# Optimization experiments

Hardware: AMD Instinct MI355X
Metric: run time of the kernel (lower is better)

The kernel has to match this reference:

```python
import jax, jax.numpy as jnp
import numpy as np


def _sample_plane(plane, coords):
    """torch.nn.functional.grid_sample, mode='bilinear', padding_mode='zeros',
    align_corners=True.  plane: [C,H,W]; coords: [N,2] with (x,y) in [-1,1]
    (x indexes W, y indexes H, as in torch grid convention).  Returns [N,C]."""
    C, H, W = plane.shape
    x = (coords[:, 0] + 1.0) * 0.5 * (W - 1)
    y = (coords[:, 1] + 1.0) * 0.5 * (H - 1)
    x0f = jnp.floor(x); y0f = jnp.floor(y)
    wx = x - x0f; wy = y - y0f

    def corner(yi, xi):
        valid = (xi >= 0) & (xi < W) & (yi >= 0) & (yi < H)
        xc = jnp.clip(xi, 0, W - 1).astype(jnp.int32)
        yc = jnp.clip(yi, 0, H - 1).astype(jnp.int32)
        return plane[:, yc, xc] * valid.astype(plane.dtype)  # [C,N]

    v00 = corner(y0f, x0f)
    v01 = corner(y0f, x0f + 1)
    v10 = corner(y0f + 1, x0f)
    v11 = corner(y0f + 1, x0f + 1)
    out = (v00 * (1 - wx) * (1 - wy) + v01 * wx * (1 - wy)
           + v10 * (1 - wx) * wy + v11 * wx * wy)
    return out.T  # [N,C]


_sample_batched = jax.vmap(_sample_plane)  # [B,C,H,W],[B,N,2] -> [B,N,C]


def setup_inputs() -> dict:
    key = jax.random.key(0)
    ks = jax.random.split(key, 8)
    B, N, C, R = 4, 131072, 32, 256
    triplanes = jax.random.normal(ks[0], (B, 3, C, R, R), jnp.float32) * 0.1
    coordinates = jax.random.uniform(ks[1], (B, N, 3), jnp.float32, -1.0, 1.0)
    # MLP weights ~ frequency_init(30) / first_layer_sine_init scales
    w0 = jax.random.uniform(ks[2], (128, C), jnp.float32, -1.0 / C, 1.0 / C)
    b0 = jnp.zeros((128,), jnp.float32)
    s1 = np.sqrt(6.0 / 128) / 30.0
    w1 = jax.random.uniform(ks[3], (128, 128), jnp.float32, -s1, s1)
    b1 = jnp.zeros((128,), jnp.float32)
    w2 = jax.random.uniform(ks[4], (1, 128), jnp.float32, -s1, s1)
    b2 = jnp.zeros((1,), jnp.float32)
    return {"triplanes": triplanes, "coordinates": coordinates,
            "w0": w0, "b0": b0, "w1": w1, "b1": b1, "w2": w2, "b2": b2}


def reference(triplanes, coordinates, w0, b0, w1, b1, w2, b2):
    # triplanes: [B,3,C,R,R]; coordinates: [B,N,3]
    xy = _sample_batched(triplanes[:, 0], coordinates[..., 0:2])   # (x,y)
    yz = _sample_batched(triplanes[:, 1], coordinates[..., 1:3])   # (y,z)
    xz = _sample_batched(triplanes[:, 2], coordinates[..., 0::2])  # (x,z)
    features = xy * yz * xz  # aggregate_fn == 'prod'; [B,N,C]
    h = jax.nn.relu(jnp.einsum('bnc,hc->bnh', features, w0) + b0)
    h = jax.nn.relu(jnp.einsum('bnh,gh->bng', h, w1) + b1)
    return jnp.einsum('bng,og->bno', h, w2) + b2  # [B,N,1]
```

## Files before the change

kernel.cpp:

```cpp
#include <hip/hip_runtime.h>
#include <hip/hip_bf16.h>
#include <cstddef>

#define RES 256
#define NCH 32
#define NPT 131072
#define NB  4

typedef _Float16 half8 __attribute__((ext_vector_type(8)));
typedef _Float16 half4 __attribute__((ext_vector_type(4)));
typedef float    f32x4 __attribute__((ext_vector_type(4)));

#define FEAT_STRIDE 40
#define H0_STRIDE   136
#define WAVE_LDS    (32 * H0_STRIDE)

__global__ __launch_bounds__(256) void transpose_prep_kernel(
    const float* __restrict__ in,
    const float* __restrict__ w0, const float* __restrict__ w1,
    _Float16* __restrict__ out,
    _Float16* __restrict__ w0h, _Float16* __restrict__ w1h)
{
    const int bp = blockIdx.y;
    const int t  = threadIdx.x;

    if (bp == 12) {
        const int i = blockIdx.x * 256 + t;
        if (i < 128 * NCH)  w0h[i] = (_Float16)(w0[i] * 16.0f);
        if (i < 128 * 128)  w1h[i] = (_Float16)w1[i];
        return;
    }

    __shared__ _Float16 tileh[NCH][RES + 8];
    const int y = blockIdx.x;

    const float4* src4 = (const float4*)(in + (size_t)bp * NCH * RES * RES);
    const int lane64 = t & 63;
    const int cq     = t >> 6;
    #pragma unroll
    for (int i = 0; i < 8; ++i) {
        const int c = cq * 8 + i;
        const float4 v = src4[(size_t)c * (RES * RES / 4) + y * (RES / 4) + lane64];
        half4 h = { (_Float16)v.x, (_Float16)v.y, (_Float16)v.z, (_Float16)v.w };
        *(half4*)&tileh[c][lane64 * 4] = h;
    }
    __syncthreads();

    _Float16* dst = out + ((size_t)bp * RES * RES + (size_t)y * RES) * NCH;
    const int x = t;
    #pragma unroll
    for (int cg = 0; cg < 4; ++cg) {
        half8 h;
        #pragma unroll
        for (int k = 0; k < 8; ++k)
            h[k] = tileh[cg * 8 + k][x];
        *(half8*)&dst[(size_t)x * NCH + cg * 8] = h;
    }
}

__global__ __launch_bounds__(64, 1) void fused_kernel(
    const _Float16* __restrict__ planesT,
    const float* __restrict__ coords,
    const _Float16* __restrict__ w0h,
    const _Float16* __restrict__ w1h,
    const float* __restrict__ b0, const float* __restrict__ b1,
    const float* __restrict__ w2, const float* __restrict__ b2,
    float* __restrict__ out)
{
    __shared__ __align__(16) _Float16 wbase[WAVE_LDS];

    const int tid  = threadIdx.x;
    const int l15  = tid & 15;
    const int quad = tid >> 4;

    {
        const int p  = tid >> 1;
        const int hf = tid & 1;
        const int gp = blockIdx.x * 32 + p;
        const int b  = gp >> 17;
        const float cx = coords[(size_t)gp * 3 + 0];
        const float cy = coords[(size_t)gp * 3 + 1];
        const float cz = coords[(size_t)gp * 3 + 2];

        int   offs[12];
        float wgt[12];
        #pragma unroll
        for (int pl = 0; pl < 3; ++pl) {
            const float u = (pl == 0) ? cx : (pl == 1) ? cy : cx;
            const float v = (pl == 0) ? cy : cz;

            const float fx = (u + 1.0f) * 0.5f * (RES - 1);
            const float fy = (v + 1.0f) * 0.5f * (RES - 1);
            const float x0f = floorf(fx), y0f = floorf(fy);
            const float wx = fx - x0f, wy = fy - y0f;
            const int x0 = (int)x0f, y0 = (int)y0f;
            const bool vx1 = (x0 + 1) < RES;
            const bool vy1 = (y0 + 1) < RES;
            const int x1 = vx1 ? x0 + 1 : RES - 1;
            const int y1 = vy1 ? y0 + 1 : RES - 1;

            float w00 = (1.0f - wx) * (1.0f - wy);
            float w01 = wx * (1.0f - wy);
            float w10 = (1.0f - wx) * wy;
            float w11 = wx * wy;
            if (!vx1) { w01 = 0.0f; w11 = 0.0f; }
            if (!vy1) { w10 = 0.0f; w11 = 0.0f; }

            const int pbase = ((b * 3 + pl) << 21) + (hf << 4);
            offs[pl * 4 + 0] = pbase + (y0 << 13) + (x0 << 5);
            offs[pl * 4 + 1] = pbase + (y0 << 13) + (x1 << 5);
            offs[pl * 4 + 2] = pbase + (y1 << 13) + (x0 << 5);
            offs[pl * 4 + 3] = pbase + (y1 << 13) + (x1 << 5);
            wgt[pl * 4 + 0] = w00; wgt[pl * 4 + 1] = w01;
            wgt[pl * 4 + 2] = w10; wgt[pl * 4 + 3] = w11;
        }

        __builtin_amdgcn_sched_barrier(0);
        half8 L0[12], L1[12];
        #pragma unroll
        for (int i = 0; i < 12; ++i) {
            const _Float16* cp = planesT + (size_t)(unsigned)offs[i];
            L0[i] = *(const half8*)cp;
            L1[i] = *(const half8*)(cp + 8);
        }
        __builtin_amdgcn_sched_barrier(0);

        float prod[16];
        #pragma unroll
        for (int pl = 0; pl < 3; ++pl) {
            #pragma unroll
            for (int k = 0; k < 8; ++k) {
                const float t0 =
                    fmaf((float)L0[pl*4+3][k], wgt[pl*4+3],
                    fmaf((float)L0[pl*4+2][k], wgt[pl*4+2],
                    fmaf((float)L0[pl*4+1][k], wgt[pl*4+1],
                         (float)L0[pl*4+0][k] * wgt[pl*4+0])));
                const float t1 =
                    fmaf((float)L1[pl*4+3][k], wgt[pl*4+3],
                    fmaf((float)L1[pl*4+2][k], wgt[pl*4+2],
                    fmaf((float)L1[pl*4+1][k], wgt[pl*4+1],
                         (float)L1[pl*4+0][k] * wgt[pl*4+0])));
                if (pl == 0) { prod[k] = t0;  prod[8 + k] = t1; }
                else         { prod[k] *= t0; prod[8 + k] *= t1; }
            }
        }

        half8 o0, o1;
        #pragma unroll
        for (int k = 0; k < 8; ++k) {
            o0[k] = (_Float16)(prod[k]     * 256.0f);
            o1[k] = (_Float16)(prod[8 + k] * 256.0f);
        }
        *(half8*)&wbase[p * FEAT_STRIDE + hf * 16 + 0] = o0;
        *(half8*)&wbase[p * FEAT_STRIDE + hf * 16 + 8] = o1;
    }

    half8 a0[2];
    #pragma unroll
    for (int mt = 0; mt < 2; ++mt)
        a0[mt] = *(const half8*)&wbase[(mt * 16 + l15) * FEAT_STRIDE + quad * 8];

    float b0v[8], b1v[8], w2s[8];
    #pragma unroll
    for (int nt = 0; nt < 8; ++nt) {
        b0v[nt] = b0[nt * 16 + l15] * 4096.0f;
        b1v[nt] = b1[nt * 16 + l15] * 4096.0f;
        w2s[nt] = w2[nt * 16 + l15] * (1.0f / 4096.0f);
    }

    #pragma unroll 1
    for (int nt = 0; nt < 8; ++nt) {
        const half8 bfr = *(const half8*)&w0h[(nt * 16 + l15) * NCH + quad * 8];
        f32x4 acc[2];
        #pragma unroll
        for (int mt = 0; mt < 2; ++mt) {
            acc[mt] = (f32x4){0.f, 0.f, 0.f, 0.f};
            acc[mt] = __builtin_amdgcn_mfma_f32_16x16x32_f16(
                a0[mt], bfr, acc[mt], 0, 0, 0);
        }
        #pragma unroll
        for (int mt = 0; mt < 2; ++mt)
            #pragma unroll
            for (int r = 0; r < 4; ++r) {
                const float hval = fmaxf(acc[mt][r] + b0v[nt], 0.0f);
                wbase[(mt * 16 + quad * 4 + r) * H0_STRIDE + nt * 16 + l15]
                    = (_Float16)hval;
            }
    }

    half8 a1[2][4];
    #pragma unroll
    for (int mt = 0; mt < 2; ++mt)
        #pragma unroll
        for (int ks = 0; ks < 4; ++ks)
            a1[mt][ks] = *(const half8*)
                &wbase[(mt * 16 + l15) * H0_STRIDE + ks * 32 + quad * 8];

    float part[2][4];
    #pragma unroll
    for (int mt = 0; mt < 2; ++mt)
        #pragma unroll
        for (int r = 0; r < 4; ++r) part[mt][r] = 0.0f;

    #pragma unroll 2
    for (int nt = 0; nt < 8; ++nt) {
        f32x4 acc[2];
        #pragma unroll
        for (int mt = 0; mt < 2; ++mt) acc[mt] = (f32x4){0.f, 0.f, 0.f, 0.f};
        #pragma unroll
        for (int ks = 0; ks < 4; ++ks) {
            const half8 bfr = *(const half8*)
                &w1h[(nt * 16 + l15) * 128 + ks * 32 + quad * 8];
            #pragma unroll
            for (int mt = 0; mt < 2; ++mt)
                acc[mt] = __builtin_amdgcn_mfma_f32_16x16x32_f16(
                    a1[mt][ks], bfr, acc[mt], 0, 0, 0);
        }
        #pragma unroll
        for (int mt = 0; mt < 2; ++mt)
            #pragma unroll
            for (int r = 0; r < 4; ++r)
                part[mt][r] = fmaf(w2s[nt], fmaxf(acc[mt][r] + b1v[nt], 0.0f),
                                   part[mt][r]);
    }

    #pragma unroll
    for (int mt = 0; mt < 2; ++mt)
        #pragma unroll
        for (int r = 0; r < 4; ++r) {
            float s = part[mt][r];
            s += __shfl_xor(s, 1);
            s += __shfl_xor(s, 2);
            s += __shfl_xor(s, 4);
            s += __shfl_xor(s, 8);
            part[mt][r] = s;
        }

    if (l15 == 0) {
        const float bias2 = b2[0];
        const int base = blockIdx.x * 32;
        #pragma unroll
        for (int mt = 0; mt < 2; ++mt)
            #pragma unroll
            for (int r = 0; r < 4; ++r)
                out[base + mt * 16 + quad * 4 + r] = part[mt][r] + bias2;
    }
}

__global__ __launch_bounds__(256) void fused_fallback(
    const float* __restrict__ planes, const float* __restrict__ coords,
    const float* __restrict__ w0, const float* __restrict__ b0,
    const float* __restrict__ w1, const float* __restrict__ b1,
    const float* __restrict__ w2, const float* __restrict__ b2,
    float* __restrict__ out)
{
    const int t = blockIdx.x * 256 + threadIdx.x;
    const int b = t >> 17;
    const float cx = coords[(size_t)t * 3 + 0];
    const float cy = coords[(size_t)t * 3 + 1];
    const float cz = coords[(size_t)t * 3 + 2];
    float feat[NCH];
    #pragma unroll
    for (int p = 0; p < 3; ++p) {
        const float u = (p == 0) ? cx : (p == 1) ? cy : cx;
        const float v = (p == 0) ? cy : cz;
        const float fx = (u + 1.0f) * 0.5f * (RES - 1);
        const float fy = (v + 1.0f) * 0.5f * (RES - 1);
        const float x0f = floorf(fx), y0f = floorf(fy);
        const float wx = fx - x0f, wy = fy - y0f;
        const int x0 = (int)x0f, y0 = (int)y0f;
        const bool vx1 = (x0 + 1) < RES, vy1 = (y0 + 1) < RES;
        const int x1 = vx1 ? x0 + 1 : RES - 1;
        const int y1 = vy1 ? y0 + 1 : RES - 1;
        float w00 = (1.0f - wx) * (1.0f - wy), w01 = wx * (1.0f - wy);
        float w10 = (1.0f - wx) * wy, w11 = wx * wy;
        if (!vx1) { w01 = 0.0f; w11 = 0.0f; }
        if (!vy1) { w10 = 0.0f; w11 = 0.0f; }
        const float* base = planes + (size_t)(b * 3 + p) * NCH * RES * RES;
        const float* p00 = base + (size_t)y0 * RES + x0;
        const float* p01 = base + (size_t)y0 * RES + x1;
        const float* p10 = base + (size_t)y1 * RES + x0;
        const float* p11 = base + (size_t)y1 * RES + x1;
        #pragma unroll
        for (int c = 0; c < NCH; ++c) {
            const size_t off = (size_t)c * RES * RES;
            float s = p00[off] * w00;
            s = fmaf(p01[off], w01, s);
            s = fmaf(p10[off], w10, s);
            s = fmaf(p11[off], w11, s);
            if (p == 0) feat[c] = s; else feat[c] *= s;
        }
    }
    float h0[128];
    #pragma unroll
    for (int g = 0; g < 128; ++g) {
        const float* wr = w0 + g * NCH;
        float aA = b0[g], aB = 0.0f;
        #pragma unroll
        for (int c = 0; c < NCH; c += 2) {
            aA = fmaf(wr[c], feat[c], aA);
            aB = fmaf(wr[c + 1], feat[c + 1], aB);
        }
        h0[g] = fmaxf(aA + aB, 0.0f);
    }
    float o = b2[0];
    for (int g = 0; g < 128; ++g) {
        const float* wr = w1 + g * 128;
        float aA = b1[g], aB = 0.0f, aC = 0.0f, aD = 0.0f;
        #pragma unroll
        for (int h = 0; h < 128; h += 4) {
            aA = fmaf(wr[h], h0[h], aA);
            aB = fmaf(wr[h + 1], h0[h + 1], aB);
            aC = fmaf(wr[h + 2], h0[h + 2], aC);
            aD = fmaf(wr[h + 3], h0[h + 3], aD);
        }
        o = fmaf(fmaxf((aA + aB) + (aC + aD), 0.0f), w2[g], o);
    }
    out[t] = o;
}

extern "C" void kernel_launch(void* const* d_in, const int* in_sizes, int n_in,
                              void* d_out, int out_size, void* d_ws, size_t ws_size,
                              hipStream_t stream)
{
    const float* trip   = (const float*)d_in[0];
    const float* coords = (const float*)d_in[1];
    const float* w0     = (const float*)d_in[2];
    const float* b0     = (const float*)d_in[3];
    const float* w1     = (const float*)d_in[4];
    const float* b1     = (const float*)d_in[5];
    const float* w2     = (const float*)d_in[6];
    const float* b2     = (const float*)d_in[7];
    float* out = (float*)d_out;

    const size_t planesTBytes = (size_t)NB * 3 * RES * RES * NCH * 2;
    const size_t w0hBytes = 128 * NCH * 2;
    const size_t w1hBytes = 128 * 128 * 2;
    const size_t needed = planesTBytes + w0hBytes + w1hBytes;

    if (ws_size >= needed) {
        _Float16* planesT = (_Float16*)d_ws;
        _Float16* w0h     = (_Float16*)((char*)d_ws + planesTBytes);
        _Float16* w1h     = (_Float16*)((char*)d_ws + planesTBytes + w0hBytes);

        transpose_prep_kernel<<<dim3(RES, NB * 3 + 1), 256, 0, stream>>>(
            trip, w0, w1, planesT, w0h, w1h);
        fused_kernel<<<(NB * NPT) / 32, 64, 0, stream>>>(
            planesT, coords, w0h, w1h, b0, b1, w2, b2, out);
    } else {
        fused_fallback<<<(NB * NPT) / 256, 256, 0, stream>>>(
            trip, coords, w0, b0, w1, b1, w2, b2, out);
    }
}
```

Before: 275.3 us.

## Split per-block points into two 16-point groups and overlap gathers with MLP

Each 64-thread block now handles its 32 points as two groups of 16, with 4 lanes per point loading 8 channels each instead of 2 lanes loading 16. Gathers for both groups are issued before the first group's interpolation and MLP, so the second group's loads can overlap compute on the first. LDS use is halved, which may help occupancy. The trade-off is that the MLP runs as single-M-tile MFMA passes, so weight fragments are reloaded twice and there is less MFMA instruction-level parallelism per pass.

Result: slower. 336.5 us (+22.2%).

```diff
diff --git a/kernel.cpp b/kernel.cpp
--- a/kernel.cpp
+++ b/kernel.cpp
@@ -13,7 +13,6 @@
 
 #define FEAT_STRIDE 40
 #define H0_STRIDE   136
-#define WAVE_LDS    (32 * H0_STRIDE)
 
 __global__ __launch_bounds__(256) void transpose_prep_kernel(
     const float* __restrict__ in,
@@ -67,23 +66,29 @@
     const float* __restrict__ w2, const float* __restrict__ b2,
     float* __restrict__ out)
 {
-    __shared__ __align__(16) _Float16 wbase[WAVE_LDS];
+    __shared__ __align__(16) _Float16 wbase[16 * H0_STRIDE];
 
     const int tid  = threadIdx.x;
     const int l15  = tid & 15;
     const int quad = tid >> 4;
-
-    {
-        const int p  = tid >> 1;
-        const int hf = tid & 1;
-        const int gp = blockIdx.x * 32 + p;
+    const int p    = tid >> 2;
+    const int hf2  = tid & 3;
+
+    float b0v[8], b1v[8], w2s[8];
+    #pragma unroll
+    for (int nt = 0; nt < 8; ++nt) {
+        b0v[nt] = b0[nt * 16 + l15] * 4096.0f;
+        b1v[nt] = b1[nt * 16 + l15] * 4096.0f;
+        w2s[nt] = w2[nt * 16 + l15] * (1.0f / 4096.0f);
+    }
+    const float bias2 = b2[0];
+
+    auto computeAddr = [&](int g, int* offs, float* wgt) {
+        const int gp = blockIdx.x * 32 + g * 16 + p;
         const int b  = gp >> 17;
         const float cx = coords[(size_t)gp * 3 + 0];
         const float cy = coords[(size_t)gp * 3 + 1];
         const float cz = coords[(size_t)gp * 3 + 2];
-
-        int   offs[12];
-        float wgt[12];
         #pragma unroll
         for (int pl = 0; pl < 3; ++pl) {
             const float u = (pl == 0) ? cx : (pl == 1) ? cy : cx;
@@ -106,7 +111,7 @@
             if (!vx1) { w01 = 0.0f; w11 = 0.0f; }
             if (!vy1) { w10 = 0.0f; w11 = 0.0f; }
 
-            const int pbase = ((b * 3 + pl) << 21) + (hf << 4);
+            const int pbase = ((b * 3 + pl) << 21) + hf2 * 8;
             offs[pl * 4 + 0] = pbase + (y0 << 13) + (x0 << 5);
             offs[pl * 4 + 1] = pbase + (y0 << 13) + (x1 << 5);
             offs[pl * 4 + 2] = pbase + (y1 << 13) + (x0 << 5);
@@ -114,137 +119,103 @@
             wgt[pl * 4 + 0] = w00; wgt[pl * 4 + 1] = w01;
             wgt[pl * 4 + 2] = w10; wgt[pl * 4 + 3] = w11;
         }
-
-        __builtin_amdgcn_sched_barrier(0);
-        half8 L0[12], L1[12];
-        #pragma unroll
-        for (int i = 0; i < 12; ++i) {
-            const _Float16* cp = planesT + (size_t)(unsigned)offs[i];
-            L0[i] = *(const half8*)cp;
-            L1[i] = *(const half8*)(cp + 8);
-        }
-        __builtin_amdgcn_sched_barrier(0);
-
-        float prod[16];
+    };
+
+    auto interpStore = [&](const half8* L, const float* wgt) {
+        float prod[8];
         #pragma unroll
         for (int pl = 0; pl < 3; ++pl) {
             #pragma unroll
             for (int k = 0; k < 8; ++k) {
                 const float t0 =
-                    fmaf((float)L0[pl*4+3][k], wgt[pl*4+3],
-                    fmaf((float)L0[pl*4+2][k], wgt[pl*4+2],
-                    fmaf((float)L0[pl*4+1][k], wgt[pl*4+1],
-                         (float)L0[pl*4+0][k] * wgt[pl*4+0])));
-                const float t1 =
-                    fmaf((float)L1[pl*4+3][k], wgt[pl*4+3],
-                    fmaf((float)L1[pl*4+2][k], wgt[pl*4+2],
-                    fmaf((float)L1[pl*4+1][k], wgt[pl*4+1],
-                         (float)L1[pl*4+0][k] * wgt[pl*4+0])));
-                if (pl == 0) { prod[k] = t0;  prod[8 + k] = t1; }
-                else         { prod[k] *= t0; prod[8 + k] *= t1; }
+                    fmaf((float)L[pl*4+3][k], wgt[pl*4+3],
+                    fmaf((float)L[pl*4+2][k], wgt[pl*4+2],
+                    fmaf((float)L[pl*4+1][k], wgt[pl*4+1],
+                         (float)L[pl*4+0][k] * wgt[pl*4+0])));
+                if (pl == 0) prod[k] = t0; else prod[k] *= t0;
             }
         }
-
-        half8 o0, o1;
-        #pragma unroll
-        for (int k = 0; k < 8; ++k) {
-            o0[k] = (_Float16)(prod[k]     * 256.0f);
-            o1[k] = (_Float16)(prod[8 + k] * 256.0f);
-        }
-        *(half8*)&wbase[p * FEAT_STRIDE + hf * 16 + 0] = o0;
-        *(half8*)&wbase[p * FEAT_STRIDE + hf * 16 + 8] = o1;
-    }
-
-    half8 a0[2];
-    #pragma unroll
-    for (int mt = 0; mt < 2; ++mt)
-        a0[mt] = *(const half8*)&wbase[(mt * 16 + l15) * FEAT_STRIDE + quad * 8];
-
-    float b0v[8], b1v[8], w2s[8];
-    #pragma unroll
-    for (int nt = 0; nt < 8; ++nt) {
-        b0v[nt] = b0[nt * 16 + l15] * 4096.0f;
-        b1v[nt] = b1[nt * 16 + l15] * 4096.0f;
-        w2s[nt] = w2[nt * 16 + l15] * (1.0f / 4096.0f);
-    }
-
-    #pragma unroll 1
-    for (int nt = 0; nt < 8; ++nt) {
-        const half8 bfr = *(const half8*)&w0h[(nt * 16 + l15) * NCH + quad * 8];
-        f32x4 acc[2];
-        #pragma unroll
-        for (int mt = 0; mt < 2; ++mt) {
-            acc[mt] = (f32x4){0.f, 0.f, 0.f, 0.f};
-            acc[mt] = __builtin_amdgcn_mfma_f32_16x16x32_f16(
-                a0[mt], bfr, acc[mt], 0, 0, 0);
-        }
-        #pragma unroll
-        for (int mt = 0; mt < 2; ++mt)
+        half8 o;
+        #pragma unroll
+        for (int k = 0; k < 8; ++k) o[k] = (_Float16)(prod[k] * 256.0f);
+        *(half8*)&wbase[p * FEAT_STRIDE + hf2 * 8] = o;
+    };
+
+    auto mlpAndOut = [&](int g) {
+        const half8 a0 = *(const half8*)&wbase[l15 * FEAT_STRIDE + quad * 8];
+
+        #pragma unroll 1
+        for (int nt = 0; nt < 8; ++nt) {
+            const half8 bfr = *(const half8*)&w0h[(nt * 16 + l15) * NCH + quad * 8];
+            f32x4 acc = (f32x4){0.f, 0.f, 0.f, 0.f};
+            acc = __builtin_amdgcn_mfma_f32_16x16x32_f16(a0, bfr, acc, 0, 0, 0);
             #pragma unroll
             for (int r = 0; r < 4; ++r) {
-                const float hval = fmaxf(acc[mt][r] + b0v[nt], 0.0f);
-                wbase[(mt * 16 + quad * 4 + r) * H0_STRIDE + nt * 16 + l15]
-                    = (_Float16)hval;
+                const float hval = fmaxf(acc[r] + b0v[nt], 0.0f);
+                wbase[(quad * 4 + r) * H0_STRIDE + nt * 16 + l15] = (_Float16)hval;
             }
-    }
-
-    half8 a1[2][4];
-    #pragma unroll
-    for (int mt = 0; mt < 2; ++mt)
+        }
+
+        half8 a1[4];
         #pragma unroll
         for (int ks = 0; ks < 4; ++ks)
-            a1[mt][ks] = *(const half8*)
-                &wbase[(mt * 16 + l15) * H0_STRIDE + ks * 32 + quad * 8];
-
-    float part[2][4];
-    #pragma unroll
-    for (int mt = 0; mt < 2; ++mt)
-        #pragma unroll
-        for (int r = 0; r < 4; ++r) part[mt][r] = 0.0f;
-
-    #pragma unroll 2
-    for (int nt = 0; nt < 8; ++nt) {
-        f32x4 acc[2];
-        #pragma unroll
-        for (int mt = 0; mt < 2; ++mt) acc[mt] = (f32x4){0.f, 0.f, 0.f, 0.f};
-        #pragma unroll
-        for (int ks = 0; ks < 4; ++ks) {
-            const half8 bfr = *(const half8*)
-                &w1h[(nt * 16 + l15) * 128 + ks * 32 + quad * 8];
-            #pragma unroll
-            for (int mt = 0; mt < 2; ++mt)
-                acc[mt] = __builtin_amdgcn_mfma_f32_16x16x32_f16(
-                    a1[mt][ks], bfr, acc[mt], 0, 0, 0);
-        }
-        #pragma unroll
-        for (int mt = 0; mt < 2; ++mt)
+            a1[ks] = *(const half8*)&wbase[l15 * H0_STRIDE + ks * 32 + quad * 8];
+
+        float part[4] = {0.f, 0.f, 0.f, 0.f};
+        #pragma unroll 2
+        for (int nt = 0; nt < 8; ++nt) {
+            f32x4 acc = (f32x4){0.f, 0.f, 0.f, 0.f};
+            #pragma unroll
+            for (int ks = 0; ks < 4; ++ks) {
+                const half8 bfr = *(const half8*)
+                    &w1h[(nt * 16 + l15) * 128 + ks * 32 + quad * 8];
+                acc = __builtin_amdgcn_mfma_f32_16x16x32_f16(a1[ks], bfr, acc, 0, 0, 0);
+            }
             #pragma unroll
             for (int r = 0; r < 4; ++r)
-                part[mt][r] = fmaf(w2s[nt], fmaxf(acc[mt][r] + b1v[nt], 0.0f),
-                                   part[mt][r]);
-    }
-
-    #pragma unroll
-    for (int mt = 0; mt < 2; ++mt)
+                part[r] = fmaf(w2s[nt], fmaxf(acc[r] + b1v[nt], 0.0f), part[r]);
+        }
+
         #pragma unroll
         for (int r = 0; r < 4; ++r) {
-            float s = part[mt][r];
+            float s = part[r];
             s += __shfl_xor(s, 1);
             s += __shfl_xor(s, 2);
             s += __shfl_xor(s, 4);
             s += __shfl_xor(s, 8);
-            part[mt][r] = s;
-        }
-
-    if (l15 == 0) {
-        const float bias2 = b2[0];
-        const int base = blockIdx.x * 32;
-        #pragma unroll
-        for (int mt = 0; mt < 2; ++mt)
+            part[r] = s;
+        }
+
+        if (l15 == 0) {
+            const int base = blockIdx.x * 32 + g * 16;
             #pragma unroll
             for (int r = 0; r < 4; ++r)
-                out[base + mt * 16 + quad * 4 + r] = part[mt][r] + bias2;
-    }
+                out[base + quad * 4 + r] = part[r] + bias2;
+        }
+    };
+
+    int offsA[12]; float wgtA[12];
+    computeAddr(0, offsA, wgtA);
+    __builtin_amdgcn_sched_barrier(0);
+    half8 LA[12];
+    #pragma unroll
+    for (int i = 0; i < 12; ++i)
+        LA[i] = *(const half8*)(planesT + (size_t)(unsigned)offsA[i]);
+    __builtin_amdgcn_sched_barrier(0);
+
+    int offsB[12]; float wgtB[12];
+    computeAddr(1, offsB, wgtB);
+    __builtin_amdgcn_sched_barrier(0);
+    half8 LB[12];
+    #pragma unroll
+    for (int i = 0; i < 12; ++i)
+        LB[i] = *(const half8*)(planesT + (size_t)(unsigned)offsB[i]);
+    __builtin_amdgcn_sched_barrier(0);
+
+    interpStore(LA, wgtA);
+    mlpAndOut(0);
+    interpStore(LB, wgtB);
+    mlpAndOut(1);
 }
 
 __global__ __launch_bounds__(256) void fused_fallback(
```

## Process two point groups per wave, prefetching second group's gathers during first MLP

Applied to the files above, without the earlier changes.

Each single-wave block now handles 64 points in two groups of 32. Both groups' 24 gather loads are issued up front, so the second group's texture-like global gathers are in flight while the first group's interpolation and MFMA MLP run. The grid is halved. This hides gather latency inside one wave, at the cost of roughly double the live vector registers for the load buffers, which may lower occupancy or cause spills.

New measurement: 283.9 us. 3.1% more time.

```diff
diff --git a/kernel.cpp b/kernel.cpp
--- a/kernel.cpp
+++ b/kernel.cpp
@@ -72,18 +72,15 @@
     const int tid  = threadIdx.x;
     const int l15  = tid & 15;
     const int quad = tid >> 4;
-
-    {
-        const int p  = tid >> 1;
-        const int hf = tid & 1;
-        const int gp = blockIdx.x * 32 + p;
+    const int p    = tid >> 1;
+    const int hf   = tid & 1;
+
+    auto computeAddr = [&](int g, int* offs, float* wgt) {
+        const int gp = blockIdx.x * 64 + g * 32 + p;
         const int b  = gp >> 17;
         const float cx = coords[(size_t)gp * 3 + 0];
         const float cy = coords[(size_t)gp * 3 + 1];
         const float cz = coords[(size_t)gp * 3 + 2];
-
-        int   offs[12];
-        float wgt[12];
         #pragma unroll
         for (int pl = 0; pl < 3; ++pl) {
             const float u = (pl == 0) ? cx : (pl == 1) ? cy : cx;
@@ -114,17 +111,9 @@
             wgt[pl * 4 + 0] = w00; wgt[pl * 4 + 1] = w01;
             wgt[pl * 4 + 2] = w10; wgt[pl * 4 + 3] = w11;
         }
-
-        __builtin_amdgcn_sched_barrier(0);
-        half8 L0[12], L1[12];
-        #pragma unroll
-        for (int i = 0; i < 12; ++i) {
-            const _Float16* cp = planesT + (size_t)(unsigned)offs[i];
-            L0[i] = *(const half8*)cp;
-            L1[i] = *(const half8*)(cp + 8);
-        }
-        __builtin_amdgcn_sched_barrier(0);
-
+    };
+
+    auto interpStore = [&](const half8* L0, const half8* L1, const float* wgt) {
         float prod[16];
         #pragma unroll
         for (int pl = 0; pl < 3; ++pl) {
@@ -144,7 +133,6 @@
                 else         { prod[k] *= t0; prod[8 + k] *= t1; }
             }
         }
-
         half8 o0, o1;
         #pragma unroll
         for (int k = 0; k < 8; ++k) {
@@ -153,12 +141,118 @@
         }
         *(half8*)&wbase[p * FEAT_STRIDE + hf * 16 + 0] = o0;
         *(half8*)&wbase[p * FEAT_STRIDE + hf * 16 + 8] = o1;
-    }
-
-    half8 a0[2];
-    #pragma unroll
-    for (int mt = 0; mt < 2; ++mt)
-        a0[mt] = *(const half8*)&wbase[(mt * 16 + l15) * FEAT_STRIDE + quad * 8];
+    };
+
+    auto mlpAndOut = [&](int g, const float* b0v, const float* b1v,
+                         const float* w2s, float bias2) {
+        half8 a0[2];
+        #pragma unroll
+        for (int mt = 0; mt < 2; ++mt)
+            a0[mt] = *(const half8*)&wbase[(mt * 16 + l15) * FEAT_STRIDE + quad * 8];
+
+        #pragma unroll 1
+        for (int nt = 0; nt < 8; ++nt) {
+            const half8 bfr = *(const half8*)&w0h[(nt * 16 + l15) * NCH + quad * 8];
+            f32x4 acc[2];
+            #pragma unroll
+            for (int mt = 0; mt < 2; ++mt) {
+                acc[mt] = (f32x4){0.f, 0.f, 0.f, 0.f};
+                acc[mt] = __builtin_amdgcn_mfma_f32_16x16x32_f16(
+                    a0[mt], bfr, acc[mt], 0, 0, 0);
+            }
+            #pragma unroll
+            for (int mt = 0; mt < 2; ++mt)
+                #pragma unroll
+                for (int r = 0; r < 4; ++r) {
+                    const float hval = fmaxf(acc[mt][r] + b0v[nt], 0.0f);
+                    wbase[(mt * 16 + quad * 4 + r) * H0_STRIDE + nt * 16 + l15]
+                        = (_Float16)hval;
+                }
+        }
+
+        half8 a1[2][4];
+        #pragma unroll
+        for (int mt = 0; mt < 2; ++mt)
+            #pragma unroll
+            for (int ks = 0; ks < 4; ++ks)
+                a1[mt][ks] = *(const half8*)
+                    &wbase[(mt * 16 + l15) * H0_STRIDE + ks * 32 + quad * 8];
+
+        float part[2][4];
+        #pragma unroll
+        for (int mt = 0; mt < 2; ++mt)
+            #pragma unroll
+            for (int r = 0; r < 4; ++r) part[mt][r] = 0.0f;
+
+        #pragma unroll 2
+        for (int nt = 0; nt < 8; ++nt) {
+            f32x4 acc[2];
+            #pragma unroll
+            for (int mt = 0; mt < 2; ++mt) acc[mt] = (f32x4){0.f, 0.f, 0.f, 0.f};
+            #pragma unroll
+            for (int ks = 0; ks < 4; ++ks) {
+                const half8 bfr = *(const half8*)
+                    &w1h[(nt * 16 + l15) * 128 + ks * 32 + quad * 8];
+                #pragma unroll
+                for (int mt = 0; mt < 2; ++mt)
+                    acc[mt] = __builtin_amdgcn_mfma_f32_16x16x32_f16(
+                        a1[mt][ks], bfr, acc[mt], 0, 0, 0);
+            }
+            #pragma unroll
+            for (int mt = 0; mt < 2; ++mt)
+                #pragma unroll
+                for (int r = 0; r < 4; ++r)
+                    part[mt][r] = fmaf(w2s[nt], fmaxf(acc[mt][r] + b1v[nt], 0.0f),
+                                       part[mt][r]);
+        }
+
+        #pragma unroll
+        for (int mt = 0; mt < 2; ++mt)
+            #pragma unroll
+            for (int r = 0; r < 4; ++r) {
+                float s = part[mt][r];
+                s += __shfl_xor(s, 1);
+                s += __shfl_xor(s, 2);
+                s += __shfl_xor(s, 4);
+                s += __shfl_xor(s, 8);
+                part[mt][r] = s;
+            }
+
+        if (l15 == 0) {
+            const int base = blockIdx.x * 64 + g * 32;
+            #pragma unroll
+            for (int mt = 0; mt < 2; ++mt)
+                #pragma unroll
+                for (int r = 0; r < 4; ++r)
+                    out[base + mt * 16 + quad * 4 + r] = part[mt][r] + bias2;
+        }
+    };
+
+    int offsA[12]; float wgtA[12];
+    computeAddr(0, offsA, wgtA);
+    __builtin_amdgcn_sched_barrier(0);
+    half8 LA0[12], LA1[12];
+    #pragma unroll
+    for (int i = 0; i < 12; ++i) {
+        const _Float16* cp = planesT + (size_t)(unsigned)offsA[i];
+        LA0[i] = *(const half8*)cp;
+        LA1[i] = *(const half8*)(cp + 8);
+    }
+    __builtin_amdgcn_sched_barrier(0);
+
+    int offsB[12]; float wgtB[12];
+    computeAddr(1, offsB, wgtB);
+    __builtin_amdgcn_sched_barrier(0);
+    half8 LB0[12], LB1[12];
+    #pragma unroll
+    for (int i = 0; i < 12; ++i) {
+        const _Float16* cp = planesT + (size_t)(unsigned)offsB[i];
+        LB0[i] = *(const half8*)cp;
+        LB1[i] = *(const half8*)(cp + 8);
+    }
+    __builtin_amdgcn_sched_barrier(0);
+
+    interpStore(LA0, LA1, wgtA);
 
     float b0v[8], b1v[8], w2s[8];
     #pragma unroll
@@ -167,84 +261,11 @@
         b1v[nt] = b1[nt * 16 + l15] * 4096.0f;
         w2s[nt] = w2[nt * 16 + l15] * (1.0f / 4096.0f);
     }
-
-    #pragma unroll 1
-    for (int nt = 0; nt < 8; ++nt) {
-        const half8 bfr = *(const half8*)&w0h[(nt * 16 + l15) * NCH + quad * 8];
-        f32x4 acc[2];
-        #pragma unroll
-        for (int mt = 0; mt < 2; ++mt) {
-            acc[mt] = (f32x4){0.f, 0.f, 0.f, 0.f};
-            acc[mt] = __builtin_amdgcn_mfma_f32_16x16x32_f16(
-                a0[mt], bfr, acc[mt], 0, 0, 0);
-        }
-        #pragma unroll
-        for (int mt = 0; mt < 2; ++mt)
-            #pragma unroll
-            for (int r = 0; r < 4; ++r) {
-                const float hval = fmaxf(acc[mt][r] + b0v[nt], 0.0f);
-                wbase[(mt * 16 + quad * 4 + r) * H0_STRIDE + nt * 16 + l15]
-                    = (_Float16)hval;
-            }
-    }
-
-    half8 a1[2][4];
-    #pragma unroll
-    for (int mt = 0; mt < 2; ++mt)
-        #pragma unroll
-        for (int ks = 0; ks < 4; ++ks)
-            a1[mt][ks] = *(const half8*)
-                &wbase[(mt * 16 + l15) * H0_STRIDE + ks * 32 + quad * 8];
-
-    float part[2][4];
-    #pragma unroll
-    for (int mt = 0; mt < 2; ++mt)
-        #pragma unroll
-        for (int r = 0; r < 4; ++r) part[mt][r] = 0.0f;
-
-    #pragma unroll 2
-    for (int nt = 0; nt < 8; ++nt) {
-        f32x4 acc[2];
-        #pragma unroll
-        for (int mt = 0; mt < 2; ++mt) acc[mt] = (f32x4){0.f, 0.f, 0.f, 0.f};
-        #pragma unroll
-        for (int ks = 0; ks < 4; ++ks) {
-            const half8 bfr = *(const half8*)
-                &w1h[(nt * 16 + l15) * 128 + ks * 32 + quad * 8];
-            #pragma unroll
-            for (int mt = 0; mt < 2; ++mt)
-                acc[mt] = __builtin_amdgcn_mfma_f32_16x16x32_f16(
-                    a1[mt][ks], bfr, acc[mt], 0, 0, 0);
-        }
-        #pragma unroll
-        for (int mt = 0; mt < 2; ++mt)
-            #pragma unroll
-            for (int r = 0; r < 4; ++r)
-                part[mt][r] = fmaf(w2s[nt], fmaxf(acc[mt][r] + b1v[nt], 0.0f),
-                                   part[mt][r]);
-    }
-
-    #pragma unroll
-    for (int mt = 0; mt < 2; ++mt)
-        #pragma unroll
-        for (int r = 0; r < 4; ++r) {
-            float s = part[mt][r];
-            s += __shfl_xor(s, 1);
-            s += __shfl_xor(s, 2);
-            s += __shfl_xor(s, 4);
-            s += __shfl_xor(s, 8);
-            part[mt][r] = s;
-        }
-
-    if (l15 == 0) {
-        const float bias2 = b2[0];
-        const int base = blockIdx.x * 32;
-        #pragma unroll
-        for (int mt = 0; mt < 2; ++mt)
-            #pragma unroll
-            for (int r = 0; r < 4; ++r)
-                out[base + mt * 16 + quad * 4 + r] = part[mt][r] + bias2;
-    }
+    const float bias2 = b2[0];
+
+    mlpAndOut(0, b0v, b1v, w2s, bias2);
+    interpStore(LB0, LB1, wgtB);
+    mlpAndOut(1, b0v, b1v, w2s, bias2);
 }
 
 __global__ __launch_bounds__(256) void fused_fallback(
@@ -345,7 +366,7 @@
 
         transpose_prep_kernel<<<dim3(RES, NB * 3 + 1), 256, 0, stream>>>(
             trip, w0, w1, planesT, w0h, w1h);
-        fused_kernel<<<(NB * NPT) / 32, 64, 0, stream>>>(
+        fused_kernel<<<(NB * NPT) / 64, 64, 0, stream>>>(
             planesT, coords, w0h, w1h, b0, b1, w2, b2, out);
     } else {
         fused_fallback<<<(NB * NPT) / 256, 256, 0, stream>>>(
```
